# Performance work log

Hardware: AMD Instinct MI355X
Metric: run time of the kernel (lower is better)

The kernel has to match this reference:

```python
import jax, jax.numpy as jnp
import numpy as np

E, D, H, O, K = 8, 1024, 4096, 1024, 2
N = 4096


def setup_inputs() -> dict:
    key = jax.random.key(0)
    ks = jax.random.split(key, 8)
    s_in = 1.0 / np.sqrt(D)
    s_h = 1.0 / np.sqrt(H)
    return {
        "x": jax.random.normal(ks[0], (N, D), dtype=jnp.float32),
        "W1": jax.random.uniform(ks[1], (E, D, H), jnp.float32, -s_in, s_in),
        "b1": jax.random.uniform(ks[2], (E, H), jnp.float32, -s_in, s_in),
        "W2": jax.random.uniform(ks[3], (E, H, O), jnp.float32, -s_h, s_h),
        "b2": jax.random.uniform(ks[4], (E, O), jnp.float32, -s_h, s_h),
        "Wg": jax.random.uniform(ks[5], (D, E), jnp.float32, -s_in, s_in),
        "bg": jax.random.uniform(ks[6], (E,), jnp.float32, -s_in, s_in),
    }


def reference(x, W1, b1, W2, b2, Wg, bg):
    # gate: [N, E] -> top-k logits and expert ids
    gate_logits = x @ Wg + bg
    topv, topi = jax.lax.top_k(gate_logits, K)          # [N, K]
    weights = jax.nn.softmax(topv, axis=-1)             # softmax over the k selected logits

    # dense all-expert MLP, then gather the selected experts per token
    h = jax.nn.relu(jnp.einsum("nd,edh->enh", x, W1) + b1[:, None, :])  # [E, N, H]
    y = jnp.einsum("enh,eho->eno", h, W2) + b2[:, None, :]              # [E, N, O]

    sel = y[topi, jnp.arange(N)[:, None]]               # [N, K, O]
    return jnp.sum(weights[..., None] * sel, axis=1)    # [N, O]
```

## Files before the change

### kernel.cpp

```cpp
#include <hip/hip_runtime.h>
#include <hip/hip_bf16.h>
#include <cstdint>

typedef __bf16 bf16;
typedef bf16 bf16x8 __attribute__((ext_vector_type(8)));
typedef bf16 bf16x4 __attribute__((ext_vector_type(4)));
typedef float f32x4 __attribute__((ext_vector_type(4)));

#define N_TOK 4096
#define DIM   1024
#define HID   4096
#define OUTD  1024
#define NEXP  8

__device__ __forceinline__ void async_copy16(const void* g, void* l) {
  __builtin_amdgcn_global_load_lds(
      (const __attribute__((address_space(1))) void*)g,
      (__attribute__((address_space(3))) void*)l, 16, 0, 0);
}

__global__ __launch_bounds__(256) void gate_kernel(
    const float* __restrict__ x, const float* __restrict__ Wg,
    const float* __restrict__ bg, int* __restrict__ topE, float* __restrict__ topW)
{
  int wave = threadIdx.x >> 6, lane = threadIdx.x & 63;
  int t = blockIdx.x * 4 + wave;
  float acc[8];
#pragma unroll
  for (int e = 0; e < 8; ++e) acc[e] = 0.f;
  const float* xrow = x + (size_t)t * DIM;
#pragma unroll
  for (int i = 0; i < DIM / 64; ++i) {
    int d = i * 64 + lane;
    float xv = xrow[d];
    float4 w0 = *(const float4*)(Wg + d * 8);
    float4 w1 = *(const float4*)(Wg + d * 8 + 4);
    acc[0] += xv * w0.x; acc[1] += xv * w0.y; acc[2] += xv * w0.z; acc[3] += xv * w0.w;
    acc[4] += xv * w1.x; acc[5] += xv * w1.y; acc[6] += xv * w1.z; acc[7] += xv * w1.w;
  }
#pragma unroll
  for (int off = 32; off > 0; off >>= 1) {
#pragma unroll
    for (int e = 0; e < 8; ++e) acc[e] += __shfl_xor(acc[e], off, 64);
  }
  if (lane == 0) {
    float l[8];
#pragma unroll
    for (int e = 0; e < 8; ++e) l[e] = acc[e] + bg[e];
    int e1 = 0;
#pragma unroll
    for (int e = 1; e < 8; ++e) if (l[e] > l[e1]) e1 = e;
    int e2 = (e1 == 0) ? 1 : 0;
#pragma unroll
    for (int e = 0; e < 8; ++e) if (e != e1 && l[e] > l[e2]) e2 = e;
    float w1 = 1.f / (1.f + __expf(l[e2] - l[e1]));
    topE[t * 2] = e1; topE[t * 2 + 1] = e2;
    topW[t * 2] = w1; topW[t * 2 + 1] = 1.f - w1;
  }
}

__global__ __launch_bounds__(256) void build_lists(
    const int* __restrict__ topE, const float* __restrict__ topW,
    int* __restrict__ cnt, int* __restrict__ tok_list, float* __restrict__ w_list,
    int* __restrict__ inv)
{
  __shared__ int lcnt[8], lbase[8];
  int tid = threadIdx.x;
  if (tid < 8) lcnt[tid] = 0;
  __syncthreads();
  int t = blockIdx.x * 256 + tid;
  int e1 = topE[2 * t], e2 = topE[2 * t + 1];
  float w1 = topW[2 * t], w2 = topW[2 * t + 1];
  int p1 = atomicAdd(&lcnt[e1], 1);
  int p2 = atomicAdd(&lcnt[e2], 1);
  __syncthreads();
  if (tid < 8) lbase[tid] = atomicAdd(&cnt[tid], lcnt[tid]);
  __syncthreads();
  int i1 = e1 * N_TOK + lbase[e1] + p1;
  int i2 = e2 * N_TOK + lbase[e2] + p2;
  tok_list[i1] = t; w_list[i1] = w1;
  tok_list[i2] = t; w_list[i2] = w2;
  inv[2 * t] = i1;
  inv[2 * t + 1] = i2;
}

__global__ void scan_kernel(const int* __restrict__ cnt, int* __restrict__ base)
{
  if (threadIdx.x == 0) {
    int s = 0;
    for (int e = 0; e < 8; ++e) { base[e] = s; s += cnt[e]; }
    base[8] = s;
  }
}

__global__ __launch_bounds__(256) void gather_cvt(
    const float* __restrict__ x, const int* __restrict__ tok_list,
    const int* __restrict__ base, bf16* __restrict__ xg)
{
  int wave = threadIdx.x >> 6, lane = threadIdx.x & 63;
  int s = blockIdx.x * 4 + wave;
  int e = 0;
#pragma unroll
  for (int i = 1; i < 8; ++i) e += (s >= base[i]);
  int tok = tok_list[e * N_TOK + (s - base[e])];
  const float4* src = (const float4*)(x + (size_t)tok * DIM);
  bf16x4* dst = (bf16x4*)(xg + (size_t)s * DIM);
#pragma unroll
  for (int i = 0; i < DIM / 256; ++i) {
    float4 v = src[i * 64 + lane];
    bf16x4 o;
    o.x = (bf16)v.x; o.y = (bf16)v.y; o.z = (bf16)v.z; o.w = (bf16)v.w;
    dst[i * 64 + lane] = o;
  }
}

__global__ __launch_bounds__(256) void transpose_cvt(
    const float* __restrict__ src, bf16* __restrict__ dst, int R, int C)
{
  __shared__ bf16 tile[64][65];
  int e = blockIdx.z;
  const float* s = src + (size_t)e * R * C;
  bf16* d = dst + (size_t)e * R * C;
  int c0 = blockIdx.x * 64, r0 = blockIdx.y * 64;
  int tid = threadIdx.x;
  int rr = tid >> 4;
  int cc = (tid & 15) * 4;
#pragma unroll
  for (int i = 0; i < 4; ++i) {
    int r = i * 16 + rr;
    float4 v = *(const float4*)(s + (size_t)(r0 + r) * C + c0 + cc);
    tile[cc + 0][r] = (bf16)v.x;
    tile[cc + 1][r] = (bf16)v.y;
    tile[cc + 2][r] = (bf16)v.z;
    tile[cc + 3][r] = (bf16)v.w;
  }
  __syncthreads();
#pragma unroll
  for (int i = 0; i < 4; ++i) {
    int ct = i * 16 + rr;
    bf16x4 o;
    o.x = tile[ct][cc + 0];
    o.y = tile[ct][cc + 1];
    o.z = tile[ct][cc + 2];
    o.w = tile[ct][cc + 3];
    *(bf16x4*)(d + (size_t)(c0 + ct) * R + r0 + cc) = o;
  }
}

__global__ __launch_bounds__(256) void gemm1_kernel(
    const bf16* __restrict__ xg, const bf16* __restrict__ W1t,
    const float* __restrict__ b1, bf16* __restrict__ hbuf,
    const int* __restrict__ cnt, const int* __restrict__ base)
{
  int e = blockIdx.z;
  int M = cnt[e];
  int mt = blockIdx.y;
  if (mt * 128 >= M) return;
  int nt = blockIdx.x;
  int b0 = base[e];

  __shared__ bf16 As[128 * 32];
  __shared__ bf16 Bs[128 * 32];

  int tid = threadIdx.x;
  int wave = tid >> 6, lane = tid & 63;

  int rA0 = wave * 32 + (lane >> 2);
  int rA1 = rA0 + 16;
  int kofs = (lane & 3) * 8;
  int lm0 = min(mt * 128 + rA0, M - 1);
  int lm1 = min(mt * 128 + rA1, M - 1);
  const bf16* gA0 = xg + (size_t)(b0 + lm0) * DIM + kofs;
  const bf16* gA1 = xg + (size_t)(b0 + lm1) * DIM + kofs;
  const bf16* gB0 = W1t + ((size_t)e * HID + nt * 128 + rA0) * DIM + kofs;
  const bf16* gB1 = W1t + ((size_t)e * HID + nt * 128 + rA1) * DIM + kofs;
  bf16* lA0 = As + (wave * 2 + 0) * 512;
  bf16* lA1 = As + (wave * 2 + 1) * 512;
  bf16* lB0 = Bs + (wave * 2 + 0) * 512;
  bf16* lB1 = Bs + (wave * 2 + 1) * 512;

  int wm = wave & 1, wn = wave >> 1;
  int quad = lane >> 4, lr = lane & 15;
  f32x4 acc[4][4] = {};

  for (int kt = 0; kt < DIM / 32; ++kt) {
    int ko = kt * 32;
    async_copy16(gA0 + ko, lA0);
    async_copy16(gA1 + ko, lA1);
    async_copy16(gB0 + ko, lB0);
    async_copy16(gB1 + ko, lB1);
    __syncthreads();
    bf16x8 af[4], bfr[4];
#pragma unroll
    for (int i = 0; i < 4; ++i)
      af[i] = *(const bf16x8*)(As + (wm * 64 + i * 16 + lr) * 32 + quad * 8);
#pragma unroll
    for (int j = 0; j < 4; ++j)
      bfr[j] = *(const bf16x8*)(Bs + (wn * 64 + j * 16 + lr) * 32 + quad * 8);
#pragma unroll
    for (int i = 0; i < 4; ++i)
#pragma unroll
      for (int j = 0; j < 4; ++j)
        acc[i][j] = __builtin_amdgcn_mfma_f32_16x16x32_bf16(af[i], bfr[j], acc[i][j], 0, 0, 0);
    __syncthreads();
  }

#pragma unroll
  for (int j = 0; j < 4; ++j) {
    int col = nt * 128 + wn * 64 + j * 16 + lr;
    float bias = b1[e * HID + col];
#pragma unroll
    for (int i = 0; i < 4; ++i) {
#pragma unroll
      for (int r = 0; r < 4; ++r) {
        int lm = mt * 128 + wm * 64 + i * 16 + quad * 4 + r;
        if (lm < M) {
          float v = acc[i][j][r] + bias;
          hbuf[(size_t)(b0 + lm) * HID + col] = (bf16)fmaxf(v, 0.f);
        }
      }
    }
  }
}

__global__ __launch_bounds__(256) void gemm2_kernel(
    const bf16* __restrict__ hbuf, const bf16* __restrict__ W2t,
    const float* __restrict__ b2, float* __restrict__ ybufA, float* __restrict__ ybufB,
    const int* __restrict__ cnt, const int* __restrict__ base)
{
  int e = blockIdx.z;
  int M = cnt[e];
  int mt = blockIdx.y;
  if (mt * 128 >= M) return;
  int nt = blockIdx.x;
  int b0 = base[e];

  __shared__ bf16 As[128 * 32];
  __shared__ bf16 Bs[128 * 32];

  int tid = threadIdx.x;
  int wave = tid >> 6, lane = tid & 63;

  int rA0 = wave * 32 + (lane >> 2);
  int rA1 = rA0 + 16;
  int kofs = (lane & 3) * 8;
  int lm0 = min(mt * 128 + rA0, M - 1);
  int lm1 = min(mt * 128 + rA1, M - 1);
  const bf16* gA0 = hbuf + (size_t)(b0 + lm0) * HID + kofs;
  const bf16* gA1 = hbuf + (size_t)(b0 + lm1) * HID + kofs;
  const bf16* gB0 = W2t + ((size_t)e * OUTD + nt * 128 + rA0) * HID + kofs;
  const bf16* gB1 = W2t + ((size_t)e * OUTD + nt * 128 + rA1) * HID + kofs;
  bf16* lA0 = As + (wave * 2 + 0) * 512;
  bf16* lA1 = As + (wave * 2 + 1) * 512;
  bf16* lB0 = Bs + (wave * 2 + 0) * 512;
  bf16* lB1 = Bs + (wave * 2 + 1) * 512;

  int wm = wave & 1, wn = wave >> 1;
  int quad = lane >> 4, lr = lane & 15;
  f32x4 acc[4][4] = {};

  for (int kt = 0; kt < HID / 32; ++kt) {
    int ko = kt * 32;
    async_copy16(gA0 + ko, lA0);
    async_copy16(gA1 + ko, lA1);
    async_copy16(gB0 + ko, lB0);
    async_copy16(gB1 + ko, lB1);
    __syncthreads();
    bf16x8 af[4], bfr[4];
#pragma unroll
    for (int i = 0; i < 4; ++i)
      af[i] = *(const bf16x8*)(As + (wm * 64 + i * 16 + lr) * 32 + quad * 8);
#pragma unroll
    for (int j = 0; j < 4; ++j)
      bfr[j] = *(const bf16x8*)(Bs + (wn * 64 + j * 16 + lr) * 32 + quad * 8);
#pragma unroll
    for (int i = 0; i < 4; ++i)
#pragma unroll
      for (int j = 0; j < 4; ++j)
        acc[i][j] = __builtin_amdgcn_mfma_f32_16x16x32_bf16(af[i], bfr[j], acc[i][j], 0, 0, 0);
    __syncthreads();
  }

#pragma unroll
  for (int j = 0; j < 4; ++j) {
    int col = nt * 128 + wn * 64 + j * 16 + lr;
    float bias = b2[e * OUTD + col];
#pragma unroll
    for (int i = 0; i < 4; ++i) {
#pragma unroll
      for (int r = 0; r < 4; ++r) {
        int lm = mt * 128 + wm * 64 + i * 16 + quad * 4 + r;
        if (lm < M) {
          int slot = b0 + lm;
          float* yr = (slot < 4096) ? (ybufA + (size_t)slot * OUTD)
                                    : (ybufB + (size_t)(slot - 4096) * OUTD);
          yr[col] = acc[i][j][r] + bias;
        }
      }
    }
  }
}

__global__ __launch_bounds__(256) void combine_kernel(
    const float* __restrict__ ybufA, const float* __restrict__ ybufB,
    const int* __restrict__ inv, const float* __restrict__ topW,
    const int* __restrict__ base, float* __restrict__ out)
{
  int wave = threadIdx.x >> 6, lane = threadIdx.x & 63;
  int t = blockIdx.x * 4 + wave;
  int i0 = inv[2 * t], i1 = inv[2 * t + 1];
  float w0 = topW[2 * t], w1 = topW[2 * t + 1];
  int s0 = base[i0 >> 12] + (i0 & (N_TOK - 1));
  int s1 = base[i1 >> 12] + (i1 & (N_TOK - 1));
  const float4* r0 = (const float4*)((s0 < 4096) ? (ybufA + (size_t)s0 * OUTD)
                                                 : (ybufB + (size_t)(s0 - 4096) * OUTD));
  const float4* r1 = (const float4*)((s1 < 4096) ? (ybufA + (size_t)s1 * OUTD)
                                                 : (ybufB + (size_t)(s1 - 4096) * OUTD));
  float4* o = (float4*)(out + (size_t)t * OUTD);
#pragma unroll
  for (int i = 0; i < OUTD / 256; ++i) {
    float4 a = r0[i * 64 + lane];
    float4 b = r1[i * 64 + lane];
    float4 c;
    c.x = w0 * a.x + w1 * b.x;
    c.y = w0 * a.y + w1 * b.y;
    c.z = w0 * a.z + w1 * b.z;
    c.w = w0 * a.w + w1 * b.w;
    o[i * 64 + lane] = c;
  }
}

extern "C" void kernel_launch(void* const* d_in, const int* in_sizes, int n_in,
                              void* d_out, int out_size, void* d_ws, size_t ws_size,
                              hipStream_t stream)
{
  (void)in_sizes; (void)n_in; (void)ws_size; (void)out_size;
  const float* x  = (const float*)d_in[0];
  const float* W1 = (const float*)d_in[1];
  const float* b1 = (const float*)d_in[2];
  const float* W2 = (const float*)d_in[3];
  const float* b2 = (const float*)d_in[4];
  const float* Wg = (const float*)d_in[5];
  const float* bg = (const float*)d_in[6];
  float* out = (float*)d_out;

  char* ws = (char*)d_ws;
  int*   tok_list = (int*)(ws + 0);
  float* w_list   = (float*)(ws + 131072);
  int*   topE     = (int*)(ws + 262144);
  float* topW     = (float*)(ws + 294912);
  int*   cnt      = (int*)(ws + 327680);
  int*   base     = (int*)(ws + 327744);
  int*   inv      = (int*)(ws + 327808);
  bf16*  xg    = (bf16*)(ws + 393216);
  bf16*  W1t   = (bf16*)(ws + 17170432);
  bf16*  hbuf  = (bf16*)(ws + 84279296);
  bf16*  W2t   = (bf16*)(ws + 393216);
  float* ybufA = (float*)(ws + 67502080);
  float* ybufB = (float*)(ws + 151388160);

  hipMemsetAsync(cnt, 0, 64, stream);

  gate_kernel<<<dim3(N_TOK / 4), 256, 0, stream>>>(x, Wg, bg, topE, topW);
  build_lists<<<dim3(N_TOK / 256), 256, 0, stream>>>(topE, topW, cnt, tok_list, w_list, inv);
  scan_kernel<<<dim3(1), 64, 0, stream>>>(cnt, base);
  gather_cvt<<<dim3(2 * N_TOK / 4), 256, 0, stream>>>(x, tok_list, base, xg);
  transpose_cvt<<<dim3(HID / 64, DIM / 64, NEXP), 256, 0, stream>>>(W1, W1t, DIM, HID);
  gemm1_kernel<<<dim3(HID / 128, N_TOK / 128, NEXP), 256, 0, stream>>>(xg, W1t, b1, hbuf, cnt, base);
  transpose_cvt<<<dim3(OUTD / 64, HID / 64, NEXP), 256, 0, stream>>>(W2, W2t, HID, OUTD);
  gemm2_kernel<<<dim3(OUTD / 128, N_TOK / 128, NEXP), 256, 0, stream>>>(hbuf, W2t, b2, ybufA, ybufB, cnt, base);
  combine_kernel<<<dim3(N_TOK / 4), 256, 0, stream>>>(ybufA, ybufB, inv, topW, base, out);
}
```

Before: 588.4 us.

## Double-buffer GEMM LDS tiles with K=64 and XOR swizzle to avoid bank conflicts

Both expert GEMM kernels now stage 64-wide K tiles into two LDS buffers, so the next tile's async global-to-LDS loads overlap the MFMA work on the current tile. This halves the number of barriers per K. An XOR swizzle on the 16-byte chunk index is applied to both the stores and the fragment reads, to reduce LDS bank conflicts. The transpose kernel pads its tile to 68 columns and reads four bf16 values as one vector. The cost is four times the LDS per block, which may lower occupancy.

```diff
diff --git a/kernel.cpp b/kernel.cpp
--- a/kernel.cpp
+++ b/kernel.cpp
@@ -17,6 +17,21 @@
   __builtin_amdgcn_global_load_lds(
       (const __attribute__((address_space(1))) void*)g,
       (__attribute__((address_space(3))) void*)l, 16, 0, 0);
+}
+
+__device__ __forceinline__ void stage_tile2(
+    const bf16* pA0, const bf16* pA1, const bf16* pA2, const bf16* pA3,
+    const bf16* pB0, const bf16* pB1, const bf16* pB2, const bf16* pB3,
+    bf16* lA, bf16* lB, int ko, int wave)
+{
+  async_copy16(pA0 + ko, lA + (wave * 4 + 0) * 512);
+  async_copy16(pA1 + ko, lA + (wave * 4 + 1) * 512);
+  async_copy16(pA2 + ko, lA + (wave * 4 + 2) * 512);
+  async_copy16(pA3 + ko, lA + (wave * 4 + 3) * 512);
+  async_copy16(pB0 + ko, lB + (wave * 4 + 0) * 512);
+  async_copy16(pB1 + ko, lB + (wave * 4 + 1) * 512);
+  async_copy16(pB2 + ko, lB + (wave * 4 + 2) * 512);
+  async_copy16(pB3 + ko, lB + (wave * 4 + 3) * 512);
 }
 
 __global__ __launch_bounds__(256) void gate_kernel(
@@ -117,7 +132,7 @@
 __global__ __launch_bounds__(256) void transpose_cvt(
     const float* __restrict__ src, bf16* __restrict__ dst, int R, int C)
 {
-  __shared__ bf16 tile[64][65];
+  __shared__ bf16 tile[64][68];
   int e = blockIdx.z;
   const float* s = src + (size_t)e * R * C;
   bf16* d = dst + (size_t)e * R * C;
@@ -138,11 +153,7 @@
 #pragma unroll
   for (int i = 0; i < 4; ++i) {
     int ct = i * 16 + rr;
-    bf16x4 o;
-    o.x = tile[ct][cc + 0];
-    o.y = tile[ct][cc + 1];
-    o.z = tile[ct][cc + 2];
-    o.w = tile[ct][cc + 3];
+    bf16x4 o = *(const bf16x4*)&tile[ct][cc];
     *(bf16x4*)(d + (size_t)(c0 + ct) * R + r0 + cc) = o;
   }
 }
@@ -159,49 +170,54 @@
   int nt = blockIdx.x;
   int b0 = base[e];
 
-  __shared__ bf16 As[128 * 32];
-  __shared__ bf16 Bs[128 * 32];
+  __shared__ bf16 As[2 * 8192];
+  __shared__ bf16 Bs[2 * 8192];
 
   int tid = threadIdx.x;
   int wave = tid >> 6, lane = tid & 63;
-
-  int rA0 = wave * 32 + (lane >> 2);
-  int rA1 = rA0 + 16;
-  int kofs = (lane & 3) * 8;
-  int lm0 = min(mt * 128 + rA0, M - 1);
-  int lm1 = min(mt * 128 + rA1, M - 1);
-  const bf16* gA0 = xg + (size_t)(b0 + lm0) * DIM + kofs;
-  const bf16* gA1 = xg + (size_t)(b0 + lm1) * DIM + kofs;
-  const bf16* gB0 = W1t + ((size_t)e * HID + nt * 128 + rA0) * DIM + kofs;
-  const bf16* gB1 = W1t + ((size_t)e * HID + nt * 128 + rA1) * DIM + kofs;
-  bf16* lA0 = As + (wave * 2 + 0) * 512;
-  bf16* lA1 = As + (wave * 2 + 1) * 512;
-  bf16* lB0 = Bs + (wave * 2 + 0) * 512;
-  bf16* lB1 = Bs + (wave * 2 + 1) * 512;
+  int crow = lane >> 3;
+  int ck   = ((lane & 7) ^ crow) * 8;
+
+  const bf16* pA[4]; const bf16* pB[4];
+#pragma unroll
+  for (int i = 0; i < 4; ++i) {
+    int ra = (wave * 4 + i) * 8 + crow;
+    int lm = min(mt * 128 + ra, M - 1);
+    pA[i] = xg + (size_t)(b0 + lm) * DIM + ck;
+    pB[i] = W1t + ((size_t)e * HID + nt * 128 + ra) * DIM + ck;
+  }
 
   int wm = wave & 1, wn = wave >> 1;
   int quad = lane >> 4, lr = lane & 15;
+  int sw = lr & 7;
   f32x4 acc[4][4] = {};
 
-  for (int kt = 0; kt < DIM / 32; ++kt) {
-    int ko = kt * 32;
-    async_copy16(gA0 + ko, lA0);
-    async_copy16(gA1 + ko, lA1);
-    async_copy16(gB0 + ko, lB0);
-    async_copy16(gB1 + ko, lB1);
-    __syncthreads();
-    bf16x8 af[4], bfr[4];
-#pragma unroll
-    for (int i = 0; i < 4; ++i)
-      af[i] = *(const bf16x8*)(As + (wm * 64 + i * 16 + lr) * 32 + quad * 8);
-#pragma unroll
-    for (int j = 0; j < 4; ++j)
-      bfr[j] = *(const bf16x8*)(Bs + (wn * 64 + j * 16 + lr) * 32 + quad * 8);
-#pragma unroll
-    for (int i = 0; i < 4; ++i)
+  const int NKT = DIM / 64;
+  stage_tile2(pA[0], pA[1], pA[2], pA[3], pB[0], pB[1], pB[2], pB[3], As, Bs, 0, wave);
+  __syncthreads();
+
+  for (int kt = 0; kt < NKT; ++kt) {
+    int cur = kt & 1;
+    if (kt + 1 < NKT)
+      stage_tile2(pA[0], pA[1], pA[2], pA[3], pB[0], pB[1], pB[2], pB[3],
+                  As + (cur ^ 1) * 8192, Bs + (cur ^ 1) * 8192, (kt + 1) * 64, wave);
+    const bf16* Asb = As + cur * 8192;
+    const bf16* Bsb = Bs + cur * 8192;
+#pragma unroll
+    for (int kk = 0; kk < 2; ++kk) {
+      bf16x8 af[4], bfr[4];
+#pragma unroll
+      for (int i = 0; i < 4; ++i)
+        af[i] = *(const bf16x8*)(Asb + (wm * 64 + i * 16 + lr) * 64 + (((kk * 4 + quad) ^ sw) * 8));
 #pragma unroll
       for (int j = 0; j < 4; ++j)
-        acc[i][j] = __builtin_amdgcn_mfma_f32_16x16x32_bf16(af[i], bfr[j], acc[i][j], 0, 0, 0);
+        bfr[j] = *(const bf16x8*)(Bsb + (wn * 64 + j * 16 + lr) * 64 + (((kk * 4 + quad) ^ sw) * 8));
+#pragma unroll
+      for (int i = 0; i < 4; ++i)
+#pragma unroll
+        for (int j = 0; j < 4; ++j)
+          acc[i][j] = __builtin_amdgcn_mfma_f32_16x16x32_bf16(af[i], bfr[j], acc[i][j], 0, 0, 0);
+    }
     __syncthreads();
   }
 
@@ -235,49 +251,54 @@
   int nt = blockIdx.x;
   int b0 = base[e];
 
-  __shared__ bf16 As[128 * 32];
-  __shared__ bf16 Bs[128 * 32];
+  __shared__ bf16 As[2 * 8192];
+  __shared__ bf16 Bs[2 * 8192];
 
   int tid = threadIdx.x;
   int wave = tid >> 6, lane = tid & 63;
-
-  int rA0 = wave * 32 + (lane >> 2);
-  int rA1 = rA0 + 16;
-  int kofs = (lane & 3) * 8;
-  int lm0 = min(mt * 128 + rA0, M - 1);
-  int lm1 = min(mt * 128 + rA1, M - 1);
-  const bf16* gA0 = hbuf + (size_t)(b0 + lm0) * HID + kofs;
-  const bf16* gA1 = hbuf + (size_t)(b0 + lm1) * HID + kofs;
-  const bf16* gB0 = W2t + ((size_t)e * OUTD + nt * 128 + rA0) * HID + kofs;
-  const bf16* gB1 = W2t + ((size_t)e * OUTD + nt * 128 + rA1) * HID + kofs;
-  bf16* lA0 = As + (wave * 2 + 0) * 512;
-  bf16* lA1 = As + (wave * 2 + 1) * 512;
-  bf16* lB0 = Bs + (wave * 2 + 0) * 512;
-  bf16* lB1 = Bs + (wave * 2 + 1) * 512;
+  int crow = lane >> 3;
+  int ck   = ((lane & 7) ^ crow) * 8;
+
+  const bf16* pA[4]; const bf16* pB[4];
+#pragma unroll
+  for (int i = 0; i < 4; ++i) {
+    int ra = (wave * 4 + i) * 8 + crow;
+    int lm = min(mt * 128 + ra, M - 1);
+    pA[i] = hbuf + (size_t)(b0 + lm) * HID + ck;
+    pB[i] = W2t + ((size_t)e * OUTD + nt * 128 + ra) * HID + ck;
+  }
 
   int wm = wave & 1, wn = wave >> 1;
   int quad = lane >> 4, lr = lane & 15;
+  int sw = lr & 7;
   f32x4 acc[4][4] = {};
 
-  for (int kt = 0; kt < HID / 32; ++kt) {
-    int ko = kt * 32;
-    async_copy16(gA0 + ko, lA0);
-    async_copy16(gA1 + ko, lA1);
-    async_copy16(gB0 + ko, lB0);
-    async_copy16(gB1 + ko, lB1);
-    __syncthreads();
-    bf16x8 af[4], bfr[4];
-#pragma unroll
-    for (int i = 0; i < 4; ++i)
-      af[i] = *(const bf16x8*)(As + (wm * 64 + i * 16 + lr) * 32 + quad * 8);
-#pragma unroll
-    for (int j = 0; j < 4; ++j)
-      bfr[j] = *(const bf16x8*)(Bs + (wn * 64 + j * 16 + lr) * 32 + quad * 8);
-#pragma unroll
-    for (int i = 0; i < 4; ++i)
+  const int NKT = HID / 64;
+  stage_tile2(pA[0], pA[1], pA[2], pA[3], pB[0], pB[1], pB[2], pB[3], As, Bs, 0, wave);
+  __syncthreads();
+
+  for (int kt = 0; kt < NKT; ++kt) {
+    int cur = kt & 1;
+    if (kt + 1 < NKT)
+      stage_tile2(pA[0], pA[1], pA[2], pA[3], pB[0], pB[1], pB[2], pB[3],
+                  As + (cur ^ 1) * 8192, Bs + (cur ^ 1) * 8192, (kt + 1) * 64, wave);
+    const bf16* Asb = As + cur * 8192;
+    const bf16* Bsb = Bs + cur * 8192;
+#pragma unroll
+    for (int kk = 0; kk < 2; ++kk) {
+      bf16x8 af[4], bfr[4];
+#pragma unroll
+      for (int i = 0; i < 4; ++i)
+        af[i] = *(const bf16x8*)(Asb + (wm * 64 + i * 16 + lr) * 64 + (((kk * 4 + quad) ^ sw) * 8));
 #pragma unroll
       for (int j = 0; j < 4; ++j)
-        acc[i][j] = __builtin_amdgcn_mfma_f32_16x16x32_bf16(af[i], bfr[j], acc[i][j], 0, 0, 0);
+        bfr[j] = *(const bf16x8*)(Bsb + (wn * 64 + j * 16 + lr) * 64 + (((kk * 4 + quad) ^ sw) * 8));
+#pragma unroll
+      for (int i = 0; i < 4; ++i)
+#pragma unroll
+        for (int j = 0; j < 4; ++j)
+          acc[i][j] = __builtin_amdgcn_mfma_f32_16x16x32_bf16(af[i], bfr[j], acc[i][j], 0, 0, 0);
+    }
     __syncthreads();
   }
 
```

New measurement: 695.0 us. +18.1%, slower.

## Swizzle GEMM LDS layout, split-K gemm2, vectorize transpose readback

Applied to the files above, without the earlier changes.

Applies an XOR swizzle to the 16-byte chunk positions in LDS for both GEMMs so the MFMA fragment reads avoid bank conflicts. When the workspace is large enough, gemm2 is split into two K halves written to separate partial buffers, and combine sums them, which doubles gemm2's grid for better CU occupancy. The transpose tile is padded to 68 so its readback can be a single vector load. Split-K adds extra fp32 partial writes and reads, and the path depends on the workspace size.

```diff
diff --git a/kernel.cpp b/kernel.cpp
--- a/kernel.cpp
+++ b/kernel.cpp
@@ -117,7 +117,7 @@
 __global__ __launch_bounds__(256) void transpose_cvt(
     const float* __restrict__ src, bf16* __restrict__ dst, int R, int C)
 {
-  __shared__ bf16 tile[64][65];
+  __shared__ bf16 tile[64][68];
   int e = blockIdx.z;
   const float* s = src + (size_t)e * R * C;
   bf16* d = dst + (size_t)e * R * C;
@@ -138,11 +138,7 @@
 #pragma unroll
   for (int i = 0; i < 4; ++i) {
     int ct = i * 16 + rr;
-    bf16x4 o;
-    o.x = tile[ct][cc + 0];
-    o.y = tile[ct][cc + 1];
-    o.z = tile[ct][cc + 2];
-    o.w = tile[ct][cc + 3];
+    bf16x4 o = *(const bf16x4*)&tile[ct][cc];
     *(bf16x4*)(d + (size_t)(c0 + ct) * R + r0 + cc) = o;
   }
 }
@@ -165,15 +161,16 @@
   int tid = threadIdx.x;
   int wave = tid >> 6, lane = tid & 63;
 
-  int rA0 = wave * 32 + (lane >> 2);
+  int rr = lane >> 2;
+  int ck = ((lane & 3) ^ (rr & 3)) * 8;
+  int rA0 = wave * 32 + rr;
   int rA1 = rA0 + 16;
-  int kofs = (lane & 3) * 8;
   int lm0 = min(mt * 128 + rA0, M - 1);
   int lm1 = min(mt * 128 + rA1, M - 1);
-  const bf16* gA0 = xg + (size_t)(b0 + lm0) * DIM + kofs;
-  const bf16* gA1 = xg + (size_t)(b0 + lm1) * DIM + kofs;
-  const bf16* gB0 = W1t + ((size_t)e * HID + nt * 128 + rA0) * DIM + kofs;
-  const bf16* gB1 = W1t + ((size_t)e * HID + nt * 128 + rA1) * DIM + kofs;
+  const bf16* gA0 = xg + (size_t)(b0 + lm0) * DIM + ck;
+  const bf16* gA1 = xg + (size_t)(b0 + lm1) * DIM + ck;
+  const bf16* gB0 = W1t + ((size_t)e * HID + nt * 128 + rA0) * DIM + ck;
+  const bf16* gB1 = W1t + ((size_t)e * HID + nt * 128 + rA1) * DIM + ck;
   bf16* lA0 = As + (wave * 2 + 0) * 512;
   bf16* lA1 = As + (wave * 2 + 1) * 512;
   bf16* lB0 = Bs + (wave * 2 + 0) * 512;
@@ -181,6 +178,7 @@
 
   int wm = wave & 1, wn = wave >> 1;
   int quad = lane >> 4, lr = lane & 15;
+  int sA = (quad ^ (lr & 3)) * 8;
   f32x4 acc[4][4] = {};
 
   for (int kt = 0; kt < DIM / 32; ++kt) {
@@ -193,10 +191,10 @@
     bf16x8 af[4], bfr[4];
 #pragma unroll
     for (int i = 0; i < 4; ++i)
-      af[i] = *(const bf16x8*)(As + (wm * 64 + i * 16 + lr) * 32 + quad * 8);
+      af[i] = *(const bf16x8*)(As + (wm * 64 + i * 16 + lr) * 32 + sA);
 #pragma unroll
     for (int j = 0; j < 4; ++j)
-      bfr[j] = *(const bf16x8*)(Bs + (wn * 64 + j * 16 + lr) * 32 + quad * 8);
+      bfr[j] = *(const bf16x8*)(Bs + (wn * 64 + j * 16 + lr) * 32 + sA);
 #pragma unroll
     for (int i = 0; i < 4; ++i)
 #pragma unroll
@@ -225,15 +223,21 @@
 
 __global__ __launch_bounds__(256) void gemm2_kernel(
     const bf16* __restrict__ hbuf, const bf16* __restrict__ W2t,
-    const float* __restrict__ b2, float* __restrict__ ybufA, float* __restrict__ ybufB,
-    const int* __restrict__ cnt, const int* __restrict__ base)
-{
-  int e = blockIdx.z;
+    const float* __restrict__ b2,
+    float* __restrict__ yA0, float* __restrict__ yB0,
+    float* __restrict__ yA1, float* __restrict__ yB1,
+    const int* __restrict__ cnt, const int* __restrict__ base, int nks)
+{
+  int z = blockIdx.z;
+  int e = z / nks;
+  int ks = z - e * nks;
   int M = cnt[e];
   int mt = blockIdx.y;
   if (mt * 128 >= M) return;
   int nt = blockIdx.x;
   int b0 = base[e];
+  int kbase = ks * (HID / nks);
+  int niter = (HID / nks) / 32;
 
   __shared__ bf16 As[128 * 32];
   __shared__ bf16 Bs[128 * 32];
@@ -241,15 +245,16 @@
   int tid = threadIdx.x;
   int wave = tid >> 6, lane = tid & 63;
 
-  int rA0 = wave * 32 + (lane >> 2);
+  int rr = lane >> 2;
+  int ck = ((lane & 3) ^ (rr & 3)) * 8;
+  int rA0 = wave * 32 + rr;
   int rA1 = rA0 + 16;
-  int kofs = (lane & 3) * 8;
   int lm0 = min(mt * 128 + rA0, M - 1);
   int lm1 = min(mt * 128 + rA1, M - 1);
-  const bf16* gA0 = hbuf + (size_t)(b0 + lm0) * HID + kofs;
-  const bf16* gA1 = hbuf + (size_t)(b0 + lm1) * HID + kofs;
-  const bf16* gB0 = W2t + ((size_t)e * OUTD + nt * 128 + rA0) * HID + kofs;
-  const bf16* gB1 = W2t + ((size_t)e * OUTD + nt * 128 + rA1) * HID + kofs;
+  const bf16* gA0 = hbuf + (size_t)(b0 + lm0) * HID + kbase + ck;
+  const bf16* gA1 = hbuf + (size_t)(b0 + lm1) * HID + kbase + ck;
+  const bf16* gB0 = W2t + ((size_t)e * OUTD + nt * 128 + rA0) * HID + kbase + ck;
+  const bf16* gB1 = W2t + ((size_t)e * OUTD + nt * 128 + rA1) * HID + kbase + ck;
   bf16* lA0 = As + (wave * 2 + 0) * 512;
   bf16* lA1 = As + (wave * 2 + 1) * 512;
   bf16* lB0 = Bs + (wave * 2 + 0) * 512;
@@ -257,9 +262,10 @@
 
   int wm = wave & 1, wn = wave >> 1;
   int quad = lane >> 4, lr = lane & 15;
+  int sA = (quad ^ (lr & 3)) * 8;
   f32x4 acc[4][4] = {};
 
-  for (int kt = 0; kt < HID / 32; ++kt) {
+  for (int kt = 0; kt < niter; ++kt) {
     int ko = kt * 32;
     async_copy16(gA0 + ko, lA0);
     async_copy16(gA1 + ko, lA1);
@@ -269,10 +275,10 @@
     bf16x8 af[4], bfr[4];
 #pragma unroll
     for (int i = 0; i < 4; ++i)
-      af[i] = *(const bf16x8*)(As + (wm * 64 + i * 16 + lr) * 32 + quad * 8);
+      af[i] = *(const bf16x8*)(As + (wm * 64 + i * 16 + lr) * 32 + sA);
 #pragma unroll
     for (int j = 0; j < 4; ++j)
-      bfr[j] = *(const bf16x8*)(Bs + (wn * 64 + j * 16 + lr) * 32 + quad * 8);
+      bfr[j] = *(const bf16x8*)(Bs + (wn * 64 + j * 16 + lr) * 32 + sA);
 #pragma unroll
     for (int i = 0; i < 4; ++i)
 #pragma unroll
@@ -281,10 +287,12 @@
     __syncthreads();
   }
 
+  float* const pa = (ks == 0) ? yA0 : yA1;
+  float* const pb = (ks == 0) ? yB0 : yB1;
 #pragma unroll
   for (int j = 0; j < 4; ++j) {
     int col = nt * 128 + wn * 64 + j * 16 + lr;
-    float bias = b2[e * OUTD + col];
+    float bias = (ks == 0) ? b2[e * OUTD + col] : 0.f;
 #pragma unroll
     for (int i = 0; i < 4; ++i) {
 #pragma unroll
@@ -292,8 +300,8 @@
         int lm = mt * 128 + wm * 64 + i * 16 + quad * 4 + r;
         if (lm < M) {
           int slot = b0 + lm;
-          float* yr = (slot < 4096) ? (ybufA + (size_t)slot * OUTD)
-                                    : (ybufB + (size_t)(slot - 4096) * OUTD);
+          float* yr = (slot < 4096) ? (pa + (size_t)slot * OUTD)
+                                    : (pb + (size_t)(slot - 4096) * OUTD);
           yr[col] = acc[i][j][r] + bias;
         }
       }
@@ -302,9 +310,10 @@
 }
 
 __global__ __launch_bounds__(256) void combine_kernel(
-    const float* __restrict__ ybufA, const float* __restrict__ ybufB,
+    const float* __restrict__ yA0, const float* __restrict__ yB0,
+    const float* __restrict__ yA1, const float* __restrict__ yB1,
     const int* __restrict__ inv, const float* __restrict__ topW,
-    const int* __restrict__ base, float* __restrict__ out)
+    const int* __restrict__ base, float* __restrict__ out, int nks)
 {
   int wave = threadIdx.x >> 6, lane = threadIdx.x & 63;
   int t = blockIdx.x * 4 + wave;
@@ -312,15 +321,25 @@
   float w0 = topW[2 * t], w1 = topW[2 * t + 1];
   int s0 = base[i0 >> 12] + (i0 & (N_TOK - 1));
   int s1 = base[i1 >> 12] + (i1 & (N_TOK - 1));
-  const float4* r0 = (const float4*)((s0 < 4096) ? (ybufA + (size_t)s0 * OUTD)
-                                                 : (ybufB + (size_t)(s0 - 4096) * OUTD));
-  const float4* r1 = (const float4*)((s1 < 4096) ? (ybufA + (size_t)s1 * OUTD)
-                                                 : (ybufB + (size_t)(s1 - 4096) * OUTD));
+  const float4* r0a = (const float4*)((s0 < 4096) ? (yA0 + (size_t)s0 * OUTD)
+                                                  : (yB0 + (size_t)(s0 - 4096) * OUTD));
+  const float4* r1a = (const float4*)((s1 < 4096) ? (yA0 + (size_t)s1 * OUTD)
+                                                  : (yB0 + (size_t)(s1 - 4096) * OUTD));
+  const float4* r0b = (const float4*)((s0 < 4096) ? (yA1 + (size_t)s0 * OUTD)
+                                                  : (yB1 + (size_t)(s0 - 4096) * OUTD));
+  const float4* r1b = (const float4*)((s1 < 4096) ? (yA1 + (size_t)s1 * OUTD)
+                                                  : (yB1 + (size_t)(s1 - 4096) * OUTD));
   float4* o = (float4*)(out + (size_t)t * OUTD);
 #pragma unroll
   for (int i = 0; i < OUTD / 256; ++i) {
-    float4 a = r0[i * 64 + lane];
-    float4 b = r1[i * 64 + lane];
+    float4 a = r0a[i * 64 + lane];
+    float4 b = r1a[i * 64 + lane];
+    if (nks == 2) {
+      float4 a2 = r0b[i * 64 + lane];
+      float4 b2v = r1b[i * 64 + lane];
+      a.x += a2.x; a.y += a2.y; a.z += a2.z; a.w += a2.w;
+      b.x += b2v.x; b.y += b2v.y; b.z += b2v.z; b.w += b2v.w;
+    }
     float4 c;
     c.x = w0 * a.x + w1 * b.x;
     c.y = w0 * a.y + w1 * b.y;
@@ -334,7 +353,7 @@
                               void* d_out, int out_size, void* d_ws, size_t ws_size,
                               hipStream_t stream)
 {
-  (void)in_sizes; (void)n_in; (void)ws_size; (void)out_size;
+  (void)in_sizes; (void)n_in; (void)out_size;
   const float* x  = (const float*)d_in[0];
   const float* W1 = (const float*)d_in[1];
   const float* b1 = (const float*)d_in[2];
@@ -356,8 +375,13 @@
   bf16*  W1t   = (bf16*)(ws + 17170432);
   bf16*  hbuf  = (bf16*)(ws + 84279296);
   bf16*  W2t   = (bf16*)(ws + 393216);
-  float* ybufA = (float*)(ws + 67502080);
-  float* ybufB = (float*)(ws + 151388160);
+  float* yA0   = (float*)(ws + 67502080);
+  float* yB0   = (float*)(ws + 151388160);
+
+  bool ks2 = (ws_size >= 201719808ULL);
+  int nks = ks2 ? 2 : 1;
+  float* yA1 = ks2 ? (float*)(ws + 168165376) : yA0;
+  float* yB1 = ks2 ? (float*)(ws + 184942592) : yB0;
 
   hipMemsetAsync(cnt, 0, 64, stream);
 
@@ -368,6 +392,7 @@
   transpose_cvt<<<dim3(HID / 64, DIM / 64, NEXP), 256, 0, stream>>>(W1, W1t, DIM, HID);
   gemm1_kernel<<<dim3(HID / 128, N_TOK / 128, NEXP), 256, 0, stream>>>(xg, W1t, b1, hbuf, cnt, base);
   transpose_cvt<<<dim3(OUTD / 64, HID / 64, NEXP), 256, 0, stream>>>(W2, W2t, HID, OUTD);
-  gemm2_kernel<<<dim3(OUTD / 128, N_TOK / 128, NEXP), 256, 0, stream>>>(hbuf, W2t, b2, ybufA, ybufB, cnt, base);
-  combine_kernel<<<dim3(N_TOK / 4), 256, 0, stream>>>(ybufA, ybufB, inv, topW, base, out);
-}
+  gemm2_kernel<<<dim3(OUTD / 128, N_TOK / 128, NEXP * nks), 256, 0, stream>>>(
+      hbuf, W2t, b2, yA0, yB0, yA1, yB1, cnt, base, nks);
+  combine_kernel<<<dim3(N_TOK / 4), 256, 0, stream>>>(yA0, yB0, yA1, yB1, inv, topW, base, out, nks);
+}
```

After: 603.7 us. 2.6% more time.

## Use 8-wave blocks in expert GEMMs and vectorize transpose tile reads

Applied to the files above, without the earlier changes.

Both expert GEMM kernels move from 4 waves to 8 waves per 128x128 tile. Each wave now owns a 32x64 sub-tile with half the accumulators and issues one async load each for A and B per k-step. This is meant to hide latency better and cut per-wave register pressure, at the cost of more block-level synchronization and less MFMA work per LDS read. The transpose tile is padded to 68 columns so the output stage can read a single aligned bf16x4 vector instead of four scalar LDS reads, which may change bank conflicts on the write side.

```diff
diff --git a/kernel.cpp b/kernel.cpp
--- a/kernel.cpp
+++ b/kernel.cpp
@@ -117,7 +117,7 @@
 __global__ __launch_bounds__(256) void transpose_cvt(
     const float* __restrict__ src, bf16* __restrict__ dst, int R, int C)
 {
-  __shared__ bf16 tile[64][65];
+  __shared__ bf16 tile[64][68];
   int e = blockIdx.z;
   const float* s = src + (size_t)e * R * C;
   bf16* d = dst + (size_t)e * R * C;
@@ -138,16 +138,12 @@
 #pragma unroll
   for (int i = 0; i < 4; ++i) {
     int ct = i * 16 + rr;
-    bf16x4 o;
-    o.x = tile[ct][cc + 0];
-    o.y = tile[ct][cc + 1];
-    o.z = tile[ct][cc + 2];
-    o.w = tile[ct][cc + 3];
+    bf16x4 o = *(const bf16x4*)&tile[ct][cc];
     *(bf16x4*)(d + (size_t)(c0 + ct) * R + r0 + cc) = o;
   }
 }
 
-__global__ __launch_bounds__(256) void gemm1_kernel(
+__global__ __launch_bounds__(512) void gemm1_kernel(
     const bf16* __restrict__ xg, const bf16* __restrict__ W1t,
     const float* __restrict__ b1, bf16* __restrict__ hbuf,
     const int* __restrict__ cnt, const int* __restrict__ base)
@@ -165,40 +161,32 @@
   int tid = threadIdx.x;
   int wave = tid >> 6, lane = tid & 63;
 
-  int rA0 = wave * 32 + (lane >> 2);
-  int rA1 = rA0 + 16;
-  int kofs = (lane & 3) * 8;
-  int lm0 = min(mt * 128 + rA0, M - 1);
-  int lm1 = min(mt * 128 + rA1, M - 1);
-  const bf16* gA0 = xg + (size_t)(b0 + lm0) * DIM + kofs;
-  const bf16* gA1 = xg + (size_t)(b0 + lm1) * DIM + kofs;
-  const bf16* gB0 = W1t + ((size_t)e * HID + nt * 128 + rA0) * DIM + kofs;
-  const bf16* gB1 = W1t + ((size_t)e * HID + nt * 128 + rA1) * DIM + kofs;
-  bf16* lA0 = As + (wave * 2 + 0) * 512;
-  bf16* lA1 = As + (wave * 2 + 1) * 512;
-  bf16* lB0 = Bs + (wave * 2 + 0) * 512;
-  bf16* lB1 = Bs + (wave * 2 + 1) * 512;
-
-  int wm = wave & 1, wn = wave >> 1;
+  int sr = wave * 16 + (lane >> 2);
+  int ko = (lane & 3) * 8;
+  int lmA = min(mt * 128 + sr, M - 1);
+  const bf16* gA = xg + (size_t)(b0 + lmA) * DIM + ko;
+  const bf16* gB = W1t + ((size_t)e * HID + nt * 128 + sr) * DIM + ko;
+  bf16* lA = As + wave * 512;
+  bf16* lB = Bs + wave * 512;
+
+  int wm = wave & 3, wn = wave >> 2;
   int quad = lane >> 4, lr = lane & 15;
-  f32x4 acc[4][4] = {};
+  f32x4 acc[2][4] = {};
 
   for (int kt = 0; kt < DIM / 32; ++kt) {
-    int ko = kt * 32;
-    async_copy16(gA0 + ko, lA0);
-    async_copy16(gA1 + ko, lA1);
-    async_copy16(gB0 + ko, lB0);
-    async_copy16(gB1 + ko, lB1);
+    int kofs = kt * 32;
+    async_copy16(gA + kofs, lA);
+    async_copy16(gB + kofs, lB);
     __syncthreads();
-    bf16x8 af[4], bfr[4];
-#pragma unroll
-    for (int i = 0; i < 4; ++i)
-      af[i] = *(const bf16x8*)(As + (wm * 64 + i * 16 + lr) * 32 + quad * 8);
+    bf16x8 af[2], bfr[4];
+#pragma unroll
+    for (int i = 0; i < 2; ++i)
+      af[i] = *(const bf16x8*)(As + (wm * 32 + i * 16 + lr) * 32 + quad * 8);
 #pragma unroll
     for (int j = 0; j < 4; ++j)
       bfr[j] = *(const bf16x8*)(Bs + (wn * 64 + j * 16 + lr) * 32 + quad * 8);
 #pragma unroll
-    for (int i = 0; i < 4; ++i)
+    for (int i = 0; i < 2; ++i)
 #pragma unroll
       for (int j = 0; j < 4; ++j)
         acc[i][j] = __builtin_amdgcn_mfma_f32_16x16x32_bf16(af[i], bfr[j], acc[i][j], 0, 0, 0);
@@ -210,10 +198,10 @@
     int col = nt * 128 + wn * 64 + j * 16 + lr;
     float bias = b1[e * HID + col];
 #pragma unroll
-    for (int i = 0; i < 4; ++i) {
+    for (int i = 0; i < 2; ++i) {
 #pragma unroll
       for (int r = 0; r < 4; ++r) {
-        int lm = mt * 128 + wm * 64 + i * 16 + quad * 4 + r;
+        int lm = mt * 128 + wm * 32 + i * 16 + quad * 4 + r;
         if (lm < M) {
           float v = acc[i][j][r] + bias;
           hbuf[(size_t)(b0 + lm) * HID + col] = (bf16)fmaxf(v, 0.f);
@@ -223,7 +211,7 @@
   }
 }
 
-__global__ __launch_bounds__(256) void gemm2_kernel(
+__global__ __launch_bounds__(512) void gemm2_kernel(
     const bf16* __restrict__ hbuf, const bf16* __restrict__ W2t,
     const float* __restrict__ b2, float* __restrict__ ybufA, float* __restrict__ ybufB,
     const int* __restrict__ cnt, const int* __restrict__ base)
@@ -241,40 +229,32 @@
   int tid = threadIdx.x;
   int wave = tid >> 6, lane = tid & 63;
 
-  int rA0 = wave * 32 + (lane >> 2);
-  int rA1 = rA0 + 16;
-  int kofs = (lane & 3) * 8;
-  int lm0 = min(mt * 128 + rA0, M - 1);
-  int lm1 = min(mt * 128 + rA1, M - 1);
-  const bf16* gA0 = hbuf + (size_t)(b0 + lm0) * HID + kofs;
-  const bf16* gA1 = hbuf + (size_t)(b0 + lm1) * HID + kofs;
-  const bf16* gB0 = W2t + ((size_t)e * OUTD + nt * 128 + rA0) * HID + kofs;
-  const bf16* gB1 = W2t + ((size_t)e * OUTD + nt * 128 + rA1) * HID + kofs;
-  bf16* lA0 = As + (wave * 2 + 0) * 512;
-  bf16* lA1 = As + (wave * 2 + 1) * 512;
-  bf16* lB0 = Bs + (wave * 2 + 0) * 512;
-  bf16* lB1 = Bs + (wave * 2 + 1) * 512;
-
-  int wm = wave & 1, wn = wave >> 1;
+  int sr = wave * 16 + (lane >> 2);
+  int ko = (lane & 3) * 8;
+  int lmA = min(mt * 128 + sr, M - 1);
+  const bf16* gA = hbuf + (size_t)(b0 + lmA) * HID + ko;
+  const bf16* gB = W2t + ((size_t)e * OUTD + nt * 128 + sr) * HID + ko;
+  bf16* lA = As + wave * 512;
+  bf16* lB = Bs + wave * 512;
+
+  int wm = wave & 3, wn = wave >> 2;
   int quad = lane >> 4, lr = lane & 15;
-  f32x4 acc[4][4] = {};
+  f32x4 acc[2][4] = {};
 
   for (int kt = 0; kt < HID / 32; ++kt) {
-    int ko = kt * 32;
-    async_copy16(gA0 + ko, lA0);
-    async_copy16(gA1 + ko, lA1);
-    async_copy16(gB0 + ko, lB0);
-    async_copy16(gB1 + ko, lB1);
+    int kofs = kt * 32;
+    async_copy16(gA + kofs, lA);
+    async_copy16(gB + kofs, lB);
     __syncthreads();
-    bf16x8 af[4], bfr[4];
-#pragma unroll
-    for (int i = 0; i < 4; ++i)
-      af[i] = *(const bf16x8*)(As + (wm * 64 + i * 16 + lr) * 32 + quad * 8);
+    bf16x8 af[2], bfr[4];
+#pragma unroll
+    for (int i = 0; i < 2; ++i)
+      af[i] = *(const bf16x8*)(As + (wm * 32 + i * 16 + lr) * 32 + quad * 8);
 #pragma unroll
     for (int j = 0; j < 4; ++j)
       bfr[j] = *(const bf16x8*)(Bs + (wn * 64 + j * 16 + lr) * 32 + quad * 8);
 #pragma unroll
-    for (int i = 0; i < 4; ++i)
+    for (int i = 0; i < 2; ++i)
 #pragma unroll
       for (int j = 0; j < 4; ++j)
         acc[i][j] = __builtin_amdgcn_mfma_f32_16x16x32_bf16(af[i], bfr[j], acc[i][j], 0, 0, 0);
@@ -286,10 +266,10 @@
     int col = nt * 128 + wn * 64 + j * 16 + lr;
     float bias = b2[e * OUTD + col];
 #pragma unroll
-    for (int i = 0; i < 4; ++i) {
+    for (int i = 0; i < 2; ++i) {
 #pragma unroll
       for (int r = 0; r < 4; ++r) {
-        int lm = mt * 128 + wm * 64 + i * 16 + quad * 4 + r;
+        int lm = mt * 128 + wm * 32 + i * 16 + quad * 4 + r;
         if (lm < M) {
           int slot = b0 + lm;
           float* yr = (slot < 4096) ? (ybufA + (size_t)slot * OUTD)
@@ -366,8 +346,8 @@
   scan_kernel<<<dim3(1), 64, 0, stream>>>(cnt, base);
   gather_cvt<<<dim3(2 * N_TOK / 4), 256, 0, stream>>>(x, tok_list, base, xg);
   transpose_cvt<<<dim3(HID / 64, DIM / 64, NEXP), 256, 0, stream>>>(W1, W1t, DIM, HID);
-  gemm1_kernel<<<dim3(HID / 128, N_TOK / 128, NEXP), 256, 0, stream>>>(xg, W1t, b1, hbuf, cnt, base);
+  gemm1_kernel<<<dim3(HID / 128, N_TOK / 128, NEXP), 512, 0, stream>>>(xg, W1t, b1, hbuf, cnt, base);
   transpose_cvt<<<dim3(OUTD / 64, HID / 64, NEXP), 256, 0, stream>>>(W2, W2t, HID, OUTD);
-  gemm2_kernel<<<dim3(OUTD / 128, N_TOK / 128, NEXP), 256, 0, stream>>>(hbuf, W2t, b2, ybufA, ybufB, cnt, base);
+  gemm2_kernel<<<dim3(OUTD / 128, N_TOK / 128, NEXP), 512, 0, stream>>>(hbuf, W2t, b2, ybufA, ybufB, cnt, base);
   combine_kernel<<<dim3(N_TOK / 4), 256, 0, stream>>>(ybufA, ybufB, inv, topW, base, out);
 }
```

Measured after the change: 587.2 us. About the same (-0.2%).
